# Kernel tuning notes

Hardware: AMD Instinct MI355X
Metric: run time of the kernel (lower is better)

The kernel has to match this reference:

```python
import jax, jax.numpy as jnp
import numpy as np
from jax import lax


def setup_inputs() -> dict:
    key = jax.random.key(0)
    k1, k2 = jax.random.split(key)
    B, C = 128, 256
    z_f = jax.random.normal(k1, (B, C, 7, 7), dtype=jnp.float32)
    x_f = jax.random.normal(k2, (B, C, 31, 31), dtype=jnp.float32)
    return {"z_f": z_f, "x_f": x_f}


def xcorr_depthwise(search, kernel):
    # search: [B, C, Hx, Wx], kernel: [B, C, Hz, Wz]
    B, C, Hx, Wx = search.shape
    _, _, Hz, Wz = kernel.shape
    s = search.reshape(1, B * C, Hx, Wx)          # [1, B*C, Hx, Wx]
    k = kernel.reshape(B * C, 1, Hz, Wz)          # [B*C, 1, Hz, Wz]
    out = lax.conv_general_dilated(
        s, k,
        window_strides=(1, 1),
        padding='VALID',
        dimension_numbers=('NCHW', 'OIHW', 'NCHW'),
        feature_group_count=B * C,
    )                                             # [1, B*C, Ho, Wo]
    Ho, Wo = Hx - Hz + 1, Wx - Wz + 1
    return out.reshape(B, C, Ho, Wo)


def reference(z_f, x_f):
    # DepthwiseRPN.forward: xcorr_depthwise(search=x_f, kernel=z_f)
    return xcorr_depthwise(x_f, z_f)
```

## Files before the change

kernel.cpp:

```cpp
#include <hip/hip_runtime.h>


#define PPB 5
#define WX 31
#define XPLANE 961
#define TDW (PPB * XPLANE)
#define PSTR 1032
#define XDW (PPB * PSTR)
#define ZOFF XDW
#define ZPLANE 49
#define ZDW (PPB * ZPLANE)
#define ZSTG 260
#define OPLANE 625
#define WO 25

typedef __attribute__((address_space(1))) const void gaddr_t;
typedef __attribute__((address_space(3))) void laddr_t;

__global__ __launch_bounds__(128, 2) void dwxcorr_kernel(
    const float* __restrict__ z, const float* __restrict__ x,
    float* __restrict__ out, int nplanes) {
  __shared__ float lds[XDW + ZSTG];

  const int tid = threadIdx.x;
  const int t = blockIdx.x;
  const int wb4 = (tid & ~63) * 4;
  const int wb1 = tid & ~63;
  const long XTOT = (long)nplanes * XPLANE;
  const long ZTOT = (long)nplanes * ZPLANE;
  const long xoff = (long)t * TDW;
  const long zoff = (long)t * ZDW;
  const long gz0 = zoff & ~3L;
  const int offz = (int)(zoff & 3);
  const int p0 = t * PPB;
  const int pmax = min(PPB, nplanes - p0);

  if (p0 + PPB < nplanes) {
#pragma unroll
    for (int c = 0; c < 11; ++c) {
      if (c < 10 || tid < 10) {
        int s = c * 512 + tid * 4;
        int p = s / PSTR;
        int r = s - p * PSTR;
        int row = r >> 5;
        int q = r & 31;
        int qq = q ^ ((row & 7) << 2);
        long g = xoff + (long)p * XPLANE + row * WX + qq;
        __builtin_amdgcn_global_load_lds((gaddr_t*)(x + g),
                                         (laddr_t*)&lds[c * 512 + wb4],
                                         16, 0, 0);
      }
    }
    if (tid < 65)
      __builtin_amdgcn_global_load_lds((gaddr_t*)(z + gz0 + tid * 4),
                                       (laddr_t*)&lds[ZOFF + wb4], 16, 0, 0);
  } else {
#pragma unroll
    for (int c = 0; c < 41; ++c) {
      int s = c * 128 + tid;
      if (s < XDW) {
        int p = s / PSTR;
        int r = s - p * PSTR;
        int row = r >> 5;
        int qq = (r & 31) ^ ((row & 7) << 2);
        if (p >= pmax) p = pmax - 1;
        if (row > 30) row = 30;
        if (qq > 30) qq = 30;
        long g = xoff + (long)p * XPLANE + row * WX + qq;
        if (g > XTOT - 1) g = XTOT - 1;
        __builtin_amdgcn_global_load_lds((gaddr_t*)(x + g),
                                         (laddr_t*)&lds[c * 128 + wb1], 4, 0, 0);
      }
    }
#pragma unroll
    for (int c = 0; c < 3; ++c) {
      int s = c * 128 + tid;
      if (s < ZSTG) {
        long gz = gz0 + s;
        if (gz > ZTOT - 1) gz = ZTOT - 1;
        __builtin_amdgcn_global_load_lds((gaddr_t*)(z + gz),
                                         (laddr_t*)&lds[ZOFF + c * 128 + wb1],
                                         4, 0, 0);
      }
    }
  }
  __syncthreads();

  const int cpp = tid / 25;
  if (tid >= PPB * 25 || cpp >= pmax) return;
  const int t25 = tid - cpp * 25;
  const int ty = t25 / 5;
  const int tx = t25 - ty * 5;
  const int tx5 = tx * 5;

  const float* zb = &lds[ZOFF + offz + cpp * ZPLANE];
  float zr[ZPLANE];
#pragma unroll
  for (int j = 0; j < ZPLANE; ++j) zr[j] = zb[j];

  float acc[5][5];
#pragma unroll
  for (int r = 0; r < 5; ++r)
#pragma unroll
    for (int j = 0; j < 5; ++j) acc[r][j] = 0.0f;

  const float* pb = &lds[cpp * PSTR];

#pragma unroll
  for (int iy = 0; iy < 11; ++iy) {
    const int row = ty * 5 + iy;
    const int rb = row << 5;
    const int f = (row & 7) << 2;
    float xr[11];
#pragma unroll
    for (int k = 0; k < 11; ++k) xr[k] = pb[rb + ((tx5 + k) ^ f)];
    const int ky_lo = (iy - 4 < 0) ? 0 : iy - 4;
    const int ky_hi = (iy < 6) ? iy : 6;
#pragma unroll
    for (int ky = 0; ky < 7; ++ky) {
      if (ky < ky_lo || ky > ky_hi) continue;
      const int orow = iy - ky;
#pragma unroll
      for (int kx = 0; kx < 7; ++kx) {
        const float zv = zr[ky * 7 + kx];
#pragma unroll
        for (int j = 0; j < 5; ++j)
          acc[orow][j] = fmaf(xr[kx + j], zv, acc[orow][j]);
      }
    }
  }

  float* ob = out + (long)(p0 + cpp) * OPLANE + (ty * 5) * WO + tx5;
#pragma unroll
  for (int r = 0; r < 5; ++r)
#pragma unroll
    for (int j = 0; j < 5; ++j) ob[r * WO + j] = acc[r][j];
}

extern "C" void kernel_launch(void* const* d_in, const int* in_sizes, int n_in,
                              void* d_out, int out_size, void* d_ws, size_t ws_size,
                              hipStream_t stream) {
  const float* z = (const float*)d_in[0];
  const float* x = (const float*)d_in[1];
  float* out = (float*)d_out;

  const int nplanes = in_sizes[0] / ZPLANE;
  const int blocks = (nplanes + PPB - 1) / PPB;

  hipLaunchKernelGGL(dwxcorr_kernel, dim3(blocks), dim3(128), 0, stream,
                     z, x, out, nplanes);
}
```

Before: 46.98 us.

## Pad LDS rows to stride 37 and align z planes for vector loads

The XOR-swizzled 32-wide row layout for the search planes in LDS is replaced by a padded row stride of 37, so inner-loop reads become plain base-plus-constant offsets without per-row XOR address math. The fast path now stages x with 4-byte global_load_lds (46 chunks) instead of 16-byte loads, which issues more load instructions. z planes are padded to stride 52 so each thread can read its filter with float4 LDS loads. The intent is to cut address ALU work and LDS bank conflicts in the compute loop, at the cost of a less efficient global-to-LDS copy.

```diff
diff --git a/kernel.cpp b/kernel.cpp
--- a/kernel.cpp
+++ b/kernel.cpp
@@ -5,12 +5,16 @@
 #define WX 31
 #define XPLANE 961
 #define TDW (PPB * XPLANE)
-#define PSTR 1032
+#define RS 37
+#define PSTR 1156
 #define XDW (PPB * PSTR)
-#define ZOFF XDW
+#define XCH 46
+#define XALLOC (XCH * 128)
+#define ZSTR 52
+#define ZB XALLOC
 #define ZPLANE 49
 #define ZDW (PPB * ZPLANE)
-#define ZSTG 260
+#define ZALLOC 384
 #define OPLANE 625
 #define WO 25
 
@@ -20,68 +24,68 @@
 __global__ __launch_bounds__(128, 2) void dwxcorr_kernel(
     const float* __restrict__ z, const float* __restrict__ x,
     float* __restrict__ out, int nplanes) {
-  __shared__ float lds[XDW + ZSTG];
+  __shared__ float lds[XALLOC + ZALLOC];
 
   const int tid = threadIdx.x;
   const int t = blockIdx.x;
+  const int wb1 = tid & ~63;
   const int wb4 = (tid & ~63) * 4;
-  const int wb1 = tid & ~63;
   const long XTOT = (long)nplanes * XPLANE;
   const long ZTOT = (long)nplanes * ZPLANE;
   const long xoff = (long)t * TDW;
   const long zoff = (long)t * ZDW;
-  const long gz0 = zoff & ~3L;
-  const int offz = (int)(zoff & 3);
   const int p0 = t * PPB;
   const int pmax = min(PPB, nplanes - p0);
 
   if (p0 + PPB < nplanes) {
+    int p = 0, rem = tid;
 #pragma unroll
-    for (int c = 0; c < 11; ++c) {
-      if (c < 10 || tid < 10) {
-        int s = c * 512 + tid * 4;
-        int p = s / PSTR;
-        int r = s - p * PSTR;
-        int row = r >> 5;
-        int q = r & 31;
-        int qq = q ^ ((row & 7) << 2);
-        long g = xoff + (long)p * XPLANE + row * WX + qq;
-        __builtin_amdgcn_global_load_lds((gaddr_t*)(x + g),
-                                         (laddr_t*)&lds[c * 512 + wb4],
-                                         16, 0, 0);
-      }
+    for (int c = 0; c < XCH; ++c) {
+      int row = rem / RS;
+      int col = rem - row * RS;
+      long g = xoff + (long)p * XPLANE + row * WX + col;
+      __builtin_amdgcn_global_load_lds((gaddr_t*)(x + g),
+                                       (laddr_t*)&lds[c * 128 + wb1], 4, 0, 0);
+      rem += 128;
+      if (rem >= PSTR) { rem -= PSTR; ++p; }
     }
-    if (tid < 65)
-      __builtin_amdgcn_global_load_lds((gaddr_t*)(z + gz0 + tid * 4),
-                                       (laddr_t*)&lds[ZOFF + wb4], 16, 0, 0);
+    if (tid < 65) {
+      int s4 = tid * 4;
+      int zp = s4 / ZSTR;
+      int zc = s4 - zp * ZSTR;
+      long g = zoff + (long)zp * ZPLANE + zc;
+      __builtin_amdgcn_global_load_lds((gaddr_t*)(z + g),
+                                       (laddr_t*)&lds[ZB + wb4], 16, 0, 0);
+    }
   } else {
 #pragma unroll
-    for (int c = 0; c < 41; ++c) {
+    for (int c = 0; c < XCH; ++c) {
       int s = c * 128 + tid;
-      if (s < XDW) {
-        int p = s / PSTR;
-        int r = s - p * PSTR;
-        int row = r >> 5;
-        int qq = (r & 31) ^ ((row & 7) << 2);
-        if (p >= pmax) p = pmax - 1;
-        if (row > 30) row = 30;
-        if (qq > 30) qq = 30;
-        long g = xoff + (long)p * XPLANE + row * WX + qq;
-        if (g > XTOT - 1) g = XTOT - 1;
-        __builtin_amdgcn_global_load_lds((gaddr_t*)(x + g),
-                                         (laddr_t*)&lds[c * 128 + wb1], 4, 0, 0);
-      }
+      int p = s / PSTR;
+      int r = s - p * PSTR;
+      int row = r / RS;
+      int col = r - row * RS;
+      if (p >= pmax) p = pmax - 1;
+      if (row > 30) row = 30;
+      if (col > 30) col = 30;
+      long g = xoff + (long)p * XPLANE + row * WX + col;
+      if (g > XTOT - 1) g = XTOT - 1;
+      __builtin_amdgcn_global_load_lds((gaddr_t*)(x + g),
+                                       (laddr_t*)&lds[c * 128 + wb1], 4, 0, 0);
     }
 #pragma unroll
     for (int c = 0; c < 3; ++c) {
       int s = c * 128 + tid;
-      if (s < ZSTG) {
-        long gz = gz0 + s;
-        if (gz > ZTOT - 1) gz = ZTOT - 1;
-        __builtin_amdgcn_global_load_lds((gaddr_t*)(z + gz),
-                                         (laddr_t*)&lds[ZOFF + c * 128 + wb1],
-                                         4, 0, 0);
-      }
+      int ss = (s > 259) ? 259 : s;
+      int zp = ss / ZSTR;
+      int zc = ss - zp * ZSTR;
+      if (zp >= pmax) zp = pmax - 1;
+      if (zc > 48) zc = 48;
+      long g = zoff + (long)zp * ZPLANE + zc;
+      if (g > ZTOT - 1) g = ZTOT - 1;
+      __builtin_amdgcn_global_load_lds((gaddr_t*)(z + g),
+                                       (laddr_t*)&lds[ZB + c * 128 + wb1],
+                                       4, 0, 0);
     }
   }
   __syncthreads();
@@ -93,10 +97,15 @@
   const int tx = t25 - ty * 5;
   const int tx5 = tx * 5;
 
-  const float* zb = &lds[ZOFF + offz + cpp * ZPLANE];
+  const float* zl = &lds[ZB + ZSTR * cpp];
   float zr[ZPLANE];
 #pragma unroll
-  for (int j = 0; j < ZPLANE; ++j) zr[j] = zb[j];
+  for (int i = 0; i < 12; ++i) {
+    float4 v = *(const float4*)(zl + 4 * i);
+    zr[4 * i + 0] = v.x; zr[4 * i + 1] = v.y;
+    zr[4 * i + 2] = v.z; zr[4 * i + 3] = v.w;
+  }
+  zr[48] = zl[48];
 
   float acc[5][5];
 #pragma unroll
@@ -104,16 +113,13 @@
 #pragma unroll
     for (int j = 0; j < 5; ++j) acc[r][j] = 0.0f;
 
-  const float* pb = &lds[cpp * PSTR];
+  const float* pb = &lds[cpp * PSTR + (ty * 5) * RS + tx5];
 
 #pragma unroll
   for (int iy = 0; iy < 11; ++iy) {
-    const int row = ty * 5 + iy;
-    const int rb = row << 5;
-    const int f = (row & 7) << 2;
     float xr[11];
 #pragma unroll
-    for (int k = 0; k < 11; ++k) xr[k] = pb[rb + ((tx5 + k) ^ f)];
+    for (int k = 0; k < 11; ++k) xr[k] = pb[iy * RS + k];
     const int ky_lo = (iy - 4 < 0) ? 0 : iy - 4;
     const int ky_hi = (iy < 6) ? iy : 6;
 #pragma unroll
```

New measurement: 52.36 us. 11.5% more time.
